# Optimization experiments

Hardware: AMD Instinct MI355X
Metric: run time of the kernel (lower is better)

The kernel has to match this reference:

```python
import jax, jax.numpy as jnp
import numpy as np

EPS = 1e-8  # torch F.cosine_similarity default eps


def setup_inputs() -> dict:
    key = jax.random.key(0)
    k1, k2 = jax.random.split(key)
    x = jax.random.normal(k1, (16384, 1024), dtype=jnp.float32)
    label = jax.random.randint(k2, (16384, 64), 0, 2).astype(jnp.int64)
    w = jnp.asarray(10.0, dtype=jnp.float32)  # nn.Parameter init_w
    b = jnp.asarray(-5.0, dtype=jnp.float32)  # nn.Parameter init_b
    return {"x": x, "label": label, "w": w, "b": b}


def reference(x, label, w, b):
    # Append the 'no-label' column for rows whose label vector is all zero.
    extra = (label.sum(axis=1) == 0).astype(label.dtype)[:, None]
    lab = jnp.concatenate([label, extra], axis=1).astype(x.dtype)  # [B, C]

    counts = lab.sum(axis=0)                  # [C] positives per centroid
    active = counts > 0                       # torch drops empty columns; we mask them

    # Centroids: mean of x over rows carrying each label (scatter-mean as GEMM).
    anchor = (lab.T @ x) / jnp.maximum(counts, 1.0)[:, None]   # [C, D]

    # Cosine similarity between every sample and every centroid.
    xn = jnp.maximum(jnp.linalg.norm(x, axis=1), EPS)          # [B]
    an = jnp.maximum(jnp.linalg.norm(anchor, axis=1), EPS)     # [C]
    cos = (x @ anchor.T) / (xn[:, None] * an[None, :])          # [B, C]

    logits = cos * w + b
    # Removing empty columns from softmax == setting their logits to -inf.
    logits = jnp.where(active[None, :], logits, -jnp.inf)
    logp = jax.nn.log_softmax(logits, axis=1)                   # [B, C]

    # Row expansion in torch duplicates sample i once per positive label j;
    # the logits row only depends on i, so CE over expanded rows is a
    # pair-weighted mean of -logp[i, j] over positive (i, j) pairs.
    n_pairs = lab.sum()
    nloss = -jnp.sum(jnp.where(lab > 0, logp, 0.0)) / n_pairs
    return nloss
```

## Files before the change

kernel.cpp:

```cpp
#include <hip/hip_runtime.h>
#include <hip/hip_bf16.h>
#include <stdint.h>

#define NROWS 16384
#define NDIM  1024
#define NLAB  64
#define NC    65
#define CPAD  80

typedef float float4v __attribute__((ext_vector_type(4)));
typedef short short8  __attribute__((ext_vector_type(8)));

static constexpr size_t SCALE_B = 0;
static constexpr size_t ACTB_B  = 320;
static constexpr size_t WSUM_B  = 400;
static constexpr size_t DONE_B  = 404;
static constexpr size_t CNTF_B  = 448;
static constexpr size_t CNTP_B  = 1024;
static constexpr size_t MASK_B  = 83968;
static constexpr size_t XN2_B   = 215040;
static constexpr size_t LFRAG_B = 280576;
static constexpr size_t BFRAG_B = 2902016;
static constexpr size_t XAF_B   = 3065856;
static constexpr size_t PART_B  = 36620288;
static constexpr size_t SLAB    = (size_t)CPAD * NDIM * 4;

__device__ __forceinline__ unsigned short bf16u(float f) {
    __hip_bfloat16 h = __float2bfloat16(f);
    return __builtin_bit_cast(unsigned short, h);
}
__device__ __forceinline__ unsigned pk2(float a, float b) {
    return (unsigned)bf16u(a) | ((unsigned)bf16u(b) << 16);
}

__global__ __launch_bounds__(256) void kA_labels(const int* __restrict__ label,
                                                 unsigned long long* __restrict__ masks,
                                                 unsigned* __restrict__ cntpart,
                                                 unsigned short* __restrict__ lfrag) {
    __shared__ unsigned cnt[NC];
    __shared__ unsigned long long smask[64];
    int t = threadIdx.x;
    int bid = blockIdx.x;
    if (t < NC) cnt[t] = 0;
    __syncthreads();
    int wave = t >> 6, lane = t & 63;
    int rowblock = bid * 64;
    unsigned creg = 0, zreg = 0;
#pragma unroll 4
    for (int p = 0; p < 16; ++p) {
        int row = rowblock + p * 4 + wave;
        int v = label[row * NLAB + lane];
        unsigned long long m = __ballot(v != 0);
        creg += (unsigned)((m >> lane) & 1ull);
        if (lane == 0) {
            masks[row] = m;
            smask[p * 4 + wave] = m;
            zreg += (m == 0ull) ? 1u : 0u;
        }
    }
    atomicAdd(&cnt[lane], creg);
    if (lane == 0 && zreg) atomicAdd(&cnt[64], zreg);
    __syncthreads();
    if (t < 80) cntpart[bid * 80 + t] = (t < NC) ? cnt[t] : 0u;
    for (int pid = t; pid < 640; pid += 256) {
        int rt2l = pid / 320, rem = pid % 320;
        int ct = rem >> 6, ln = rem & 63;
        int qq = ln >> 4, cc = ln & 15;
        int c = ct * 16 + cc;
        int rbase = rt2l * 32 + qq * 8;
        unsigned pk[4];
#pragma unroll
        for (int jp = 0; jp < 4; ++jp) {
            unsigned long long m0 = smask[rbase + jp * 2], m1 = smask[rbase + jp * 2 + 1];
            unsigned b0, b1;
            if (c < 64)       { b0 = (unsigned)((m0 >> c) & 1ull); b1 = (unsigned)((m1 >> c) & 1ull); }
            else if (c == 64) { b0 = (m0 == 0ull); b1 = (m1 == 0ull); }
            else              { b0 = 0u; b1 = 0u; }
            pk[jp] = (b0 ? 0x3F80u : 0u) | (b1 ? 0x3F800000u : 0u);
        }
        uint4 w = make_uint4(pk[0], pk[1], pk[2], pk[3]);
        ((uint4*)lfrag)[((size_t)(bid * 2 + rt2l) * 5 + ct) * 64 + ln] = w;
    }
}

__global__ __launch_bounds__(256) void kBP(const float* __restrict__ x,
                                           const unsigned short* __restrict__ lfrag,
                                           float* __restrict__ partial,
                                           unsigned short* __restrict__ xAfrag,
                                           float* __restrict__ xn2g,
                                           int kslices) {
    __shared__ float xt[2][32][65];
    __shared__ float red2[4][16];
    int t = threadIdx.x, wave = t >> 6, lane = t & 63;
    int q = lane >> 4, col = lane & 15;
    int ngemm = 16 * kslices;

    if ((int)blockIdx.x >= ngemm) {
        int rt = blockIdx.x - ngemm;
        const float* rowp = x + ((size_t)rt * 16 + col) * NDIM;
        uint4* dst = (uint4*)xAfrag + ((size_t)rt * 32 + wave * 8) * 64 + lane;
        float4 fa[8], fb[8];
#pragma unroll
        for (int kb = 0; kb < 8; ++kb) {
            int d0 = wave * 256 + kb * 32 + q * 8;
            fa[kb] = *(const float4*)(rowp + d0);
            fb[kb] = *(const float4*)(rowp + d0 + 4);
        }
        float sq = 0.f;
#pragma unroll
        for (int kb = 0; kb < 8; ++kb) {
            sq += fa[kb].x * fa[kb].x + fa[kb].y * fa[kb].y + fa[kb].z * fa[kb].z + fa[kb].w * fa[kb].w
                + fb[kb].x * fb[kb].x + fb[kb].y * fb[kb].y + fb[kb].z * fb[kb].z + fb[kb].w * fb[kb].w;
            uint4 v;
            v.x = pk2(fa[kb].x, fa[kb].y); v.y = pk2(fa[kb].z, fa[kb].w);
            v.z = pk2(fb[kb].x, fb[kb].y); v.w = pk2(fb[kb].z, fb[kb].w);
            dst[kb * 64] = v;
        }
        sq += __shfl_xor(sq, 16, 64);
        sq += __shfl_xor(sq, 32, 64);
        if (q == 0) red2[wave][col] = sq;
        __syncthreads();
        if (t < 16) xn2g[rt * 16 + t] = red2[0][t] + red2[1][t] + red2[2][t] + red2[3][t];
        return;
    }

    int dgroup = blockIdx.x & 15, ks = blockIdx.x >> 4;
    int nkb = (NROWS / kslices) >> 5;
    int kb0 = ks * nkb;
    int d = dgroup * 64 + wave * 16 + col;
    const uint4* A = (const uint4*)lfrag;
    int srow = t >> 3, sd = (t & 7) * 8;

    float4v acc[5];
#pragma unroll
    for (int ct = 0; ct < 5; ++ct) acc[ct] = (float4v){0.f, 0.f, 0.f, 0.f};

    {
        const float* g = x + ((size_t)(kb0 * 32 + srow)) * NDIM + dgroup * 64 + sd;
        float4 u = *(const float4*)g, v2 = *(const float4*)(g + 4);
        float* L = &xt[0][srow][sd];
        L[0] = u.x; L[1] = u.y; L[2] = u.z; L[3] = u.w;
        L[4] = v2.x; L[5] = v2.y; L[6] = v2.z; L[7] = v2.w;
    }
    __syncthreads();

    for (int i = 0; i < nkb; ++i) {
        int cur = i & 1;
        float4 u, v2;
        bool havenext = (i + 1) < nkb;
        if (havenext) {
            const float* g = x + ((size_t)((kb0 + i + 1) * 32 + srow)) * NDIM + dgroup * 64 + sd;
            u = *(const float4*)g; v2 = *(const float4*)(g + 4);
        }
        int kb = kb0 + i;
        uint4 a0[5];
#pragma unroll
        for (int ct = 0; ct < 5; ++ct) a0[ct] = A[((size_t)kb * 5 + ct) * 64 + lane];
        float f[8];
#pragma unroll
        for (int j = 0; j < 8; ++j) f[j] = xt[cur][q * 8 + j][wave * 16 + col];
        uint4 bq;
        bq.x = pk2(f[0], f[1]); bq.y = pk2(f[2], f[3]);
        bq.z = pk2(f[4], f[5]); bq.w = pk2(f[6], f[7]);
        short8 bf = __builtin_bit_cast(short8, bq);
#pragma unroll
        for (int ct = 0; ct < 5; ++ct) {
            short8 af = __builtin_bit_cast(short8, a0[ct]);
            acc[ct] = __builtin_amdgcn_mfma_f32_16x16x32_bf16(af, bf, acc[ct], 0, 0, 0);
        }
        if (havenext) {
            float* L = &xt[cur ^ 1][srow][sd];
            L[0] = u.x; L[1] = u.y; L[2] = u.z; L[3] = u.w;
            L[4] = v2.x; L[5] = v2.y; L[6] = v2.z; L[7] = v2.w;
        }
        __syncthreads();
    }
    float* pb = partial + (size_t)ks * CPAD * NDIM;
#pragma unroll
    for (int ct = 0; ct < 5; ++ct)
#pragma unroll
        for (int reg = 0; reg < 4; ++reg)
            pb[(size_t)(ct * 16 + q * 4 + reg) * NDIM + d] = acc[ct][reg];
}

__global__ __launch_bounds__(1024) void kC_fuse(const float* __restrict__ wptr,
                                                const unsigned* __restrict__ cntpart,
                                                const float* __restrict__ partial,
                                                int kslices,
                                                unsigned short* __restrict__ bfrag,
                                                float* __restrict__ scale,
                                                unsigned char* __restrict__ actB,
                                                unsigned* __restrict__ countsF,
                                                float* __restrict__ wsum,
                                                unsigned* __restrict__ done) {
    int c = blockIdx.x, t = threadIdx.x;
    __shared__ float red[16];
    __shared__ unsigned credu[4];
    __shared__ float bcast[1];
    if (c == 0 && t == 512) *wsum = 0.f;
    if (c == 0 && t == 513) *done = 0u;
    if (t < 256) {
        unsigned cv = cntpart[t * 80 + c];
#pragma unroll
        for (int m = 32; m >= 1; m >>= 1) cv += __shfl_xor(cv, m, 64);
        if ((t & 63) == 0) credu[t >> 6] = cv;
    }
    const float* p = partial + (size_t)c * NDIM + t;
    float s = 0.f;
#pragma unroll 8
    for (int sl = 0; sl < kslices; ++sl) s += p[(size_t)sl * CPAD * NDIM];
    float ss = s * s;
#pragma unroll
    for (int m = 32; m >= 1; m >>= 1) ss += __shfl_xor(ss, m, 64);
    if ((t & 63) == 0) red[t >> 6] = ss;
    __syncthreads();
    if (t == 0) {
        float tot = 0.f;
#pragma unroll
        for (int j = 0; j < 16; ++j) tot += red[j];
        bcast[0] = sqrtf(tot);
    }
    unsigned cnt = credu[0] + credu[1] + credu[2] + credu[3];
    __syncthreads();
    float invc = 1.0f / (float)(cnt > 0u ? cnt : 1u);
    float a = s * invc;
    float an = fmaxf(bcast[0] * invc, 1e-8f);
    unsigned short h = bf16u(a / an);
    int ct = c >> 4, colc = c & 15;
    int kb = t >> 5, q = (t >> 3) & 3, j0 = t & 7;
    bfrag[((((size_t)ct * 32 + kb) * 64) + q * 16 + colc) * 8 + j0] = h;
    float hv = __bfloat162float(__builtin_bit_cast(__hip_bfloat16, h));
    float nb2 = hv * hv;
#pragma unroll
    for (int m = 32; m >= 1; m >>= 1) nb2 += __shfl_xor(nb2, m, 64);
    if ((t & 63) == 0) red[t >> 6] = nb2;
    __syncthreads();
    if (t == 0) {
        float n2 = 0.f;
#pragma unroll
        for (int j = 0; j < 16; ++j) n2 += red[j];
        scale[c] = (n2 > 0.f) ? (wptr[0] / sqrtf(n2)) : 0.f;
        actB[c] = (cnt > 0u) ? 1 : 0;
        countsF[c] = cnt;
    }
}

__global__ __launch_bounds__(256) void k3_loss(const unsigned short* __restrict__ xAfrag,
                                               const unsigned short* __restrict__ bfrag,
                                               const float* __restrict__ xn2g,
                                               const unsigned long long* __restrict__ masks,
                                               const unsigned char* __restrict__ actB,
                                               const float* __restrict__ scale,
                                               const float* __restrict__ bptr,
                                               float* __restrict__ wsum,
                                               unsigned* __restrict__ done,
                                               const unsigned* __restrict__ countsF,
                                               float* __restrict__ out) {
    __shared__ float redsm[3][64][21];
    int t = threadIdx.x, wave = t >> 6, lane = t & 63;
    int q = lane >> 4, col = lane & 15;
    int rt = blockIdx.x;
    int rowbase = rt * 16;
    const uint4* A = (const uint4*)xAfrag + (size_t)rt * 32 * 64 + lane;
    const uint4* Bp = (const uint4*)bfrag + lane;
    int kb0 = wave * 8;

    float4v acc[5];
#pragma unroll
    for (int ct = 0; ct < 5; ++ct) acc[ct] = (float4v){0.f, 0.f, 0.f, 0.f};

    uint4 a[8];
#pragma unroll
    for (int j = 0; j < 8; ++j) a[j] = A[(size_t)(kb0 + j) * 64];
    uint4 b0[5], b1[5];
#pragma unroll
    for (int ct = 0; ct < 5; ++ct) b0[ct] = Bp[(size_t)(ct * 32 + kb0 + 0) * 64];
#pragma unroll
    for (int ct = 0; ct < 5; ++ct) b1[ct] = Bp[(size_t)(ct * 32 + kb0 + 1) * 64];

    for (int s = 0; s < 8; s += 2) {
        int p2 = s + 2 < 8 ? kb0 + s + 2 : kb0 + s;
        int p3 = s + 3 < 8 ? kb0 + s + 3 : kb0 + s + 1;
        {
            short8 af = __builtin_bit_cast(short8, a[s]);
#pragma unroll
            for (int ct = 0; ct < 5; ++ct) {
                short8 bf = __builtin_bit_cast(short8, b0[ct]);
                acc[ct] = __builtin_amdgcn_mfma_f32_16x16x32_bf16(af, bf, acc[ct], 0, 0, 0);
            }
#pragma unroll
            for (int ct = 0; ct < 5; ++ct) b0[ct] = Bp[(size_t)(ct * 32 + p2) * 64];
        }
        {
            short8 af = __builtin_bit_cast(short8, a[s + 1]);
#pragma unroll
            for (int ct = 0; ct < 5; ++ct) {
                short8 bf = __builtin_bit_cast(short8, b1[ct]);
                acc[ct] = __builtin_amdgcn_mfma_f32_16x16x32_bf16(af, bf, acc[ct], 0, 0, 0);
            }
#pragma unroll
            for (int ct = 0; ct < 5; ++ct) b1[ct] = Bp[(size_t)(ct * 32 + p3) * 64];
        }
    }

    if (wave) {
#pragma unroll
        for (int ct = 0; ct < 5; ++ct)
#pragma unroll
            for (int reg = 0; reg < 4; ++reg)
                redsm[wave - 1][lane][ct * 4 + reg] = acc[ct][reg];
    }
    __syncthreads();
    if (wave != 0) return;
#pragma unroll
    for (int w = 0; w < 3; ++w)
#pragma unroll
        for (int ct = 0; ct < 5; ++ct)
#pragma unroll
            for (int reg = 0; reg < 4; ++reg)
                acc[ct][reg] += redsm[w][lane][ct * 4 + reg];

    float bv = bptr[0];
    float sc[5]; unsigned char ab[5];
#pragma unroll
    for (int ct = 0; ct < 5; ++ct) { sc[ct] = scale[ct * 16 + col]; ab[ct] = actB[ct * 16 + col]; }

    float contrib = 0.f;
#pragma unroll
    for (int reg = 0; reg < 4; ++reg) {
        int rl = q * 4 + reg;
        int row = rowbase + rl;
        float inv = 1.0f / fmaxf(sqrtf(xn2g[row]), 1e-8f);
        unsigned long long mask = masks[row];
        float v[5]; float lmax = -1e30f;
#pragma unroll
        for (int ct = 0; ct < 5; ++ct) {
            float lg = acc[ct][reg] * sc[ct] * inv + bv;
            v[ct] = ab[ct] ? lg : -1e30f;
            lmax = fmaxf(lmax, v[ct]);
        }
#pragma unroll
        for (int m = 1; m < 16; m <<= 1) lmax = fmaxf(lmax, __shfl_xor(lmax, m, 16));
        float es = 0.f;
#pragma unroll
        for (int ct = 0; ct < 5; ++ct) es += expf(v[ct] - lmax);
#pragma unroll
        for (int m = 1; m < 16; m <<= 1) es += __shfl_xor(es, m, 16);
        float lse = lmax + logf(es);
        float ps = 0.f;
#pragma unroll
        for (int ct = 0; ct < 5; ++ct) {
            int c = ct * 16 + col;
            bool pos = (c < 64) ? (((mask >> c) & 1ull) != 0ull)
                                : ((c == 64) ? (mask == 0ull) : false);
            ps += pos ? v[ct] : 0.f;
        }
#pragma unroll
        for (int m = 1; m < 16; m <<= 1) ps += __shfl_xor(ps, m, 16);
        float npos = mask ? (float)__popcll(mask) : 1.0f;
        float crow = ps - npos * lse;
        if (col == 0) contrib += crow;
    }
#pragma unroll
    for (int m = 1; m < 64; m <<= 1) contrib += __shfl_xor(contrib, m, 64);
    if (lane == 0) {
        atomicAdd(wsum, contrib);
        asm volatile("s_waitcnt vmcnt(0)" ::: "memory");
        unsigned prev = atomicAdd(done, 1u);
        if (prev == (unsigned)gridDim.x - 1u) {
            float wv = __hip_atomic_load(wsum, __ATOMIC_ACQUIRE, __HIP_MEMORY_SCOPE_AGENT);
            float np = 0.f;
            for (int c = 0; c < NC; ++c) np += (float)countsF[c];
            out[0] = -wv / np;
        }
    }
}

extern "C" void kernel_launch(void* const* d_in, const int* in_sizes, int n_in,
                              void* d_out, int out_size, void* d_ws, size_t ws_size,
                              hipStream_t stream) {
    (void)in_sizes; (void)n_in; (void)out_size;
    const float* x = (const float*)d_in[0];
    const int* label = (const int*)d_in[1];
    const float* w = (const float*)d_in[2];
    const float* b = (const float*)d_in[3];

    char* ws = (char*)d_ws;
    float* scale = (float*)(ws + SCALE_B);
    unsigned char* actB = (unsigned char*)(ws + ACTB_B);
    float* wsum = (float*)(ws + WSUM_B);
    unsigned* done = (unsigned*)(ws + DONE_B);
    unsigned* countsF = (unsigned*)(ws + CNTF_B);
    unsigned* cntpart = (unsigned*)(ws + CNTP_B);
    unsigned long long* masks = (unsigned long long*)(ws + MASK_B);
    float* xn2g = (float*)(ws + XN2_B);
    unsigned short* lfrag = (unsigned short*)(ws + LFRAG_B);
    unsigned short* bfrag = (unsigned short*)(ws + BFRAG_B);
    unsigned short* xAfrag = (unsigned short*)(ws + XAF_B);
    float* partial = (float*)(ws + PART_B);

    int kslices = 64;
    while (kslices > 8 && PART_B + (size_t)kslices * SLAB > ws_size) kslices >>= 1;

    hipLaunchKernelGGL(kA_labels, dim3(256), dim3(256), 0, stream,
                       label, masks, cntpart, lfrag);
    hipLaunchKernelGGL(kBP, dim3(16 * kslices + 1024), dim3(256), 0, stream,
                       x, lfrag, partial, xAfrag, xn2g, kslices);
    hipLaunchKernelGGL(kC_fuse, dim3(CPAD), dim3(1024), 0, stream,
                       w, cntpart, partial, kslices, bfrag, scale, actB, countsF, wsum, done);
    hipLaunchKernelGGL(k3_loss, dim3(NROWS / 16), dim3(256), 0, stream,
                       xAfrag, bfrag, xn2g, masks, actB, scale, b, wsum, done, countsF, (float*)d_out);
}
```

Measured before the change: 172.1 us.

## Emit bf16 x fragments from GEMM tile loop and compute row norms in loss kernel

Removes the 1024 extra blocks that re-read x to build bf16 A-fragments and row norms. The centroid GEMM kernel now packs the staged shared-memory tile into the xAfrag layout as it goes. The loss kernel computes squared row norms from the bf16 fragments it already loads. Fast exp/log intrinsics replace expf/logf. This saves a full extra read of x (64MB), at the cost of norms computed from bf16-rounded values, which slightly changes precision.

Measured after the change: 182.9 us. 1.06x slower.

```diff
diff --git a/kernel.cpp b/kernel.cpp
--- a/kernel.cpp
+++ b/kernel.cpp
@@ -18,7 +18,6 @@
 static constexpr size_t CNTF_B  = 448;
 static constexpr size_t CNTP_B  = 1024;
 static constexpr size_t MASK_B  = 83968;
-static constexpr size_t XN2_B   = 215040;
 static constexpr size_t LFRAG_B = 280576;
 static constexpr size_t BFRAG_B = 2902016;
 static constexpr size_t XAF_B   = 3065856;
@@ -83,53 +82,27 @@
     }
 }
 
-__global__ __launch_bounds__(256) void kBP(const float* __restrict__ x,
-                                           const unsigned short* __restrict__ lfrag,
-                                           float* __restrict__ partial,
-                                           unsigned short* __restrict__ xAfrag,
-                                           float* __restrict__ xn2g,
-                                           int kslices) {
+__global__ __launch_bounds__(256) void kG(const float* __restrict__ x,
+                                          const unsigned short* __restrict__ lfrag,
+                                          float* __restrict__ partial,
+                                          unsigned short* __restrict__ xAfrag,
+                                          int kslices) {
     __shared__ float xt[2][32][65];
-    __shared__ float red2[4][16];
     int t = threadIdx.x, wave = t >> 6, lane = t & 63;
     int q = lane >> 4, col = lane & 15;
-    int ngemm = 16 * kslices;
-
-    if ((int)blockIdx.x >= ngemm) {
-        int rt = blockIdx.x - ngemm;
-        const float* rowp = x + ((size_t)rt * 16 + col) * NDIM;
-        uint4* dst = (uint4*)xAfrag + ((size_t)rt * 32 + wave * 8) * 64 + lane;
-        float4 fa[8], fb[8];
-#pragma unroll
-        for (int kb = 0; kb < 8; ++kb) {
-            int d0 = wave * 256 + kb * 32 + q * 8;
-            fa[kb] = *(const float4*)(rowp + d0);
-            fb[kb] = *(const float4*)(rowp + d0 + 4);
-        }
-        float sq = 0.f;
-#pragma unroll
-        for (int kb = 0; kb < 8; ++kb) {
-            sq += fa[kb].x * fa[kb].x + fa[kb].y * fa[kb].y + fa[kb].z * fa[kb].z + fa[kb].w * fa[kb].w
-                + fb[kb].x * fb[kb].x + fb[kb].y * fb[kb].y + fb[kb].z * fb[kb].z + fb[kb].w * fb[kb].w;
-            uint4 v;
-            v.x = pk2(fa[kb].x, fa[kb].y); v.y = pk2(fa[kb].z, fa[kb].w);
-            v.z = pk2(fb[kb].x, fb[kb].y); v.w = pk2(fb[kb].z, fb[kb].w);
-            dst[kb * 64] = v;
-        }
-        sq += __shfl_xor(sq, 16, 64);
-        sq += __shfl_xor(sq, 32, 64);
-        if (q == 0) red2[wave][col] = sq;
-        __syncthreads();
-        if (t < 16) xn2g[rt * 16 + t] = red2[0][t] + red2[1][t] + red2[2][t] + red2[3][t];
-        return;
-    }
-
     int dgroup = blockIdx.x & 15, ks = blockIdx.x >> 4;
     int nkb = (NROWS / kslices) >> 5;
     int kb0 = ks * nkb;
     int d = dgroup * 64 + wave * 16 + col;
     const uint4* A = (const uint4*)lfrag;
     int srow = t >> 3, sd = (t & 7) * 8;
+
+    int rh = t >> 7;
+    int kbh = (t >> 6) & 1;
+    int qq = (t >> 4) & 3;
+    int cc = t & 15;
+    int r2 = rh * 16 + cc;
+    int dch = kbh * 4 + qq;
 
     float4v acc[5];
 #pragma unroll
@@ -167,6 +140,16 @@
         for (int ct = 0; ct < 5; ++ct) {
             short8 af = __builtin_bit_cast(short8, a0[ct]);
             acc[ct] = __builtin_amdgcn_mfma_f32_16x16x32_bf16(af, bf, acc[ct], 0, 0, 0);
+        }
+        {
+            float g0[8];
+#pragma unroll
+            for (int j = 0; j < 8; ++j) g0[j] = xt[cur][r2][dch * 8 + j];
+            uint4 v;
+            v.x = pk2(g0[0], g0[1]); v.y = pk2(g0[2], g0[3]);
+            v.z = pk2(g0[4], g0[5]); v.w = pk2(g0[6], g0[7]);
+            size_t slot = (((size_t)kb * 2 + rh) * 32 + dgroup * 2 + kbh) * 64 + (t & 63);
+            ((uint4*)xAfrag)[slot] = v;
         }
         if (havenext) {
             float* L = &xt[cur ^ 1][srow][sd];
@@ -247,7 +230,6 @@
 
 __global__ __launch_bounds__(256) void k3_loss(const unsigned short* __restrict__ xAfrag,
                                                const unsigned short* __restrict__ bfrag,
-                                               const float* __restrict__ xn2g,
                                                const unsigned long long* __restrict__ masks,
                                                const unsigned char* __restrict__ actB,
                                                const float* __restrict__ scale,
@@ -257,6 +239,7 @@
                                                const unsigned* __restrict__ countsF,
                                                float* __restrict__ out) {
     __shared__ float redsm[3][64][21];
+    __shared__ float sqred[4][16];
     int t = threadIdx.x, wave = t >> 6, lane = t & 63;
     int q = lane >> 4, col = lane & 15;
     int rt = blockIdx.x;
@@ -278,6 +261,22 @@
 #pragma unroll
     for (int ct = 0; ct < 5; ++ct) b1[ct] = Bp[(size_t)(ct * 32 + kb0 + 1) * 64];
 
+    float sq = 0.f;
+#pragma unroll
+    for (int j = 0; j < 8; ++j) {
+        const unsigned* dw = (const unsigned*)&a[j];
+#pragma unroll
+        for (int e = 0; e < 4; ++e) {
+            float lo = __builtin_bit_cast(float, dw[e] << 16);
+            float hi = __builtin_bit_cast(float, dw[e] & 0xffff0000u);
+            sq = fmaf(lo, lo, sq);
+            sq = fmaf(hi, hi, sq);
+        }
+    }
+    sq += __shfl_xor(sq, 16, 64);
+    sq += __shfl_xor(sq, 32, 64);
+    if (lane < 16) sqred[wave][lane] = sq;
+
     for (int s = 0; s < 8; s += 2) {
         int p2 = s + 2 < 8 ? kb0 + s + 2 : kb0 + s;
         int p3 = s + 3 < 8 ? kb0 + s + 3 : kb0 + s + 1;
@@ -330,7 +329,8 @@
     for (int reg = 0; reg < 4; ++reg) {
         int rl = q * 4 + reg;
         int row = rowbase + rl;
-        float inv = 1.0f / fmaxf(sqrtf(xn2g[row]), 1e-8f);
+        float xn2v = sqred[0][rl] + sqred[1][rl] + sqred[2][rl] + sqred[3][rl];
+        float inv = 1.0f / fmaxf(sqrtf(xn2v), 1e-8f);
         unsigned long long mask = masks[row];
         float v[5]; float lmax = -1e30f;
 #pragma unroll
@@ -343,10 +343,10 @@
         for (int m = 1; m < 16; m <<= 1) lmax = fmaxf(lmax, __shfl_xor(lmax, m, 16));
         float es = 0.f;
 #pragma unroll
-        for (int ct = 0; ct < 5; ++ct) es += expf(v[ct] - lmax);
+        for (int ct = 0; ct < 5; ++ct) es += __expf(v[ct] - lmax);
 #pragma unroll
         for (int m = 1; m < 16; m <<= 1) es += __shfl_xor(es, m, 16);
-        float lse = lmax + logf(es);
+        float lse = lmax + __logf(es);
         float ps = 0.f;
 #pragma unroll
         for (int ct = 0; ct < 5; ++ct) {
@@ -393,7 +393,6 @@
     unsigned* countsF = (unsigned*)(ws + CNTF_B);
     unsigned* cntpart = (unsigned*)(ws + CNTP_B);
     unsigned long long* masks = (unsigned long long*)(ws + MASK_B);
-    float* xn2g = (float*)(ws + XN2_B);
     unsigned short* lfrag = (unsigned short*)(ws + LFRAG_B);
     unsigned short* bfrag = (unsigned short*)(ws + BFRAG_B);
     unsigned short* xAfrag = (unsigned short*)(ws + XAF_B);
@@ -404,10 +403,10 @@
 
     hipLaunchKernelGGL(kA_labels, dim3(256), dim3(256), 0, stream,
                        label, masks, cntpart, lfrag);
-    hipLaunchKernelGGL(kBP, dim3(16 * kslices + 1024), dim3(256), 0, stream,
-                       x, lfrag, partial, xAfrag, xn2g, kslices);
+    hipLaunchKernelGGL(kG, dim3(16 * kslices), dim3(256), 0, stream,
+                       x, lfrag, partial, xAfrag, kslices);
     hipLaunchKernelGGL(kC_fuse, dim3(CPAD), dim3(1024), 0, stream,
                        w, cntpart, partial, kslices, bfrag, scale, actB, countsF, wsum, done);
     hipLaunchKernelGGL(k3_loss, dim3(NROWS / 16), dim3(256), 0, stream,
-                       xAfrag, bfrag, xn2g, masks, actB, scale, b, wsum, done, countsF, (float*)d_out);
-}
+                       xAfrag, bfrag, masks, actB, scale, b, wsum, done, countsF, (float*)d_out);
+}
```
